# Optimization experiments

Hardware: AMD Instinct MI355X
Metric: run time of the kernel (lower is better)

The kernel has to match this reference:

```python
import jax, jax.numpy as jnp
import numpy as np

B, S, D, H = 8, 1024, 1024, 16
HD = D // H
EPS = 1e-5

def _layer_norm(x, g, b):
    m = jnp.mean(x, axis=-1, keepdims=True)
    v = jnp.var(x, axis=-1, keepdims=True)
    return (x - m) * jax.lax.rsqrt(v + EPS) * g + b

def setup_inputs() -> dict:
    key = jax.random.key(0)
    ks = jax.random.split(key, 12)
    s = lambda fan: 1.0 / np.sqrt(fan)
    return {
        "x": jax.random.normal(ks[0], (B, S, D), jnp.float32),
        "W_qkv": jax.random.normal(ks[1], (3 * D, D), jnp.float32) * s(D),
        "b_qkv": jnp.zeros((3 * D,), jnp.float32),
        "W_out": jax.random.normal(ks[2], (D, D), jnp.float32) * s(D),
        "b_out": jnp.zeros((D,), jnp.float32),
        "W1": jax.random.normal(ks[3], (2 * D, D), jnp.float32) * s(D),
        "b1": jnp.zeros((2 * D,), jnp.float32),
        "W2": jax.random.normal(ks[4], (D, 2 * D), jnp.float32) * s(2 * D),
        "b2": jnp.zeros((D,), jnp.float32),
        "ln1_g": jnp.ones((D,), jnp.float32),
        "ln1_b": jnp.zeros((D,), jnp.float32),
        "ln2_g": jnp.ones((D,), jnp.float32),
        "ln2_b": jnp.zeros((D,), jnp.float32),
    }

def reference(x, W_qkv, b_qkv, W_out, b_out, W1, b1, W2, b2, ln1_g, ln1_b, ln2_g, ln2_b):
    # --- self-attention (explicit, need_weights=True path) ---
    qkv = x @ W_qkv.T + b_qkv                       # [B,S,3D]
    q, k, v = jnp.split(qkv, 3, axis=-1)
    q = q.reshape(B, S, H, HD) * (1.0 / np.sqrt(HD))
    k = k.reshape(B, S, H, HD)
    v = v.reshape(B, S, H, HD)
    scores = jnp.einsum("bqhd,bkhd->bhqk", q, k)    # [B,H,S,S]
    probs = jax.nn.softmax(scores, axis=-1)          # materialized attn weights
    ctx = jnp.einsum("bhqk,bkhd->bqhd", probs, v).reshape(B, S, D)
    attn_out = ctx @ W_out.T + b_out
    # --- residual + LN, FFN, residual + LN ---
    x1 = _layer_norm(x + attn_out, ln1_g, ln1_b)
    ff = jax.nn.relu(x1 @ W1.T + b1) @ W2.T + b2
    x2 = _layer_norm(x1 + ff, ln2_g, ln2_b)
    return x2, probs
```

## Files before the change

kernel.cpp:

```cpp
#include <hip/hip_runtime.h>
#include <cstdint>

#define NB 8
#define NS 1024
#define ND 1024
#define NH 16
#define HD 64
static constexpr float LN_EPS = 1e-5f;

typedef unsigned short u16;
typedef short s16x8 __attribute__((ext_vector_type(8)));
typedef short s16x4 __attribute__((ext_vector_type(4)));
typedef float fx4   __attribute__((ext_vector_type(4)));

__device__ __forceinline__ u16 f2bf(float f) {
  union { float f; unsigned u; } v; v.f = f;
  return (u16)((v.u + 0x7fffu + ((v.u >> 16) & 1u)) >> 16);
}

__device__ __forceinline__ void gl_lds16(const void* g, void* lds) {
  __builtin_amdgcn_global_load_lds(
      (const __attribute__((address_space(1))) void*)g,
      (__attribute__((address_space(3))) void*)lds, 16, 0, 0);
}

__global__ __launch_bounds__(256) void cvt_f32_bf16(const float* __restrict__ in,
                                                    u16* __restrict__ out, int n4) {
  for (int i = blockIdx.x * 256 + threadIdx.x; i < n4; i += gridDim.x * 256) {
    const float4 v = reinterpret_cast<const float4*>(in)[i];
    s16x4 o;
    o[0] = (short)f2bf(v.x); o[1] = (short)f2bf(v.y);
    o[2] = (short)f2bf(v.z); o[3] = (short)f2bf(v.w);
    reinterpret_cast<s16x4*>(out)[i] = o;
  }
}

enum { EPI_SCORES = 0, EPI_QKV = 1, EPI_BIASRES = 2, EPI_FF1 = 3 };

template <int EPI>
__global__ __launch_bounds__(256, 2) void gemm_bt(
    const u16* __restrict__ A, const u16* __restrict__ B,
    const float* __restrict__ bias, const float* __restrict__ res,
    float* __restrict__ outF, u16* __restrict__ outB,
    u16* __restrict__ outQ, u16* __restrict__ outK, u16* __restrict__ outV,
    int M, int N, int K, long zsA, long zsB, long zsC) {
  __shared__ u16 sA[2][128 * 32];
  __shared__ u16 sB[2][128 * 32];
  const int t = threadIdx.x;
  const int lane = t & 63, wid = t >> 6;
  const int wm = wid >> 1, wn = wid & 1;
  const int z = blockIdx.z;
  A += (long)z * zsA;
  B += (long)z * zsB;
  const int tm0 = blockIdx.y * 128, tn0 = blockIdx.x * 128;
  const int nk = K >> 5;

  fx4 acc[4][4];
  const fx4 vzero = {0.f, 0.f, 0.f, 0.f};
#pragma unroll
  for (int i = 0; i < 4; ++i)
#pragma unroll
    for (int j = 0; j < 4; ++j) acc[i][j] = vzero;

  auto stage = [&](int buf, int kt) {
    const int k0 = kt << 5;
#pragma unroll
    for (int i = 0; i < 2; ++i) {
      const int e = (i * 256 + t) * 8;
      const int row = e >> 5, col = e & 31;
      gl_lds16(A + (long)(tm0 + row) * K + k0 + col, &sA[buf][e]);
    }
#pragma unroll
    for (int i = 0; i < 2; ++i) {
      const int e = (i * 256 + t) * 8;
      const int row = e >> 5, col = e & 31;
      gl_lds16(B + (long)(tn0 + row) * K + k0 + col, &sB[buf][e]);
    }
  };

  stage(0, 0);
  for (int kt = 0; kt < nk; ++kt) {
    const int cur = kt & 1;
    __syncthreads();
    if (kt + 1 < nk) stage(cur ^ 1, kt + 1);
    const int ar = wm * 64 + (lane & 15);
    const int br = wn * 64 + (lane & 15);
    const int kc = (lane >> 4) * 8;
    s16x8 a[4], b[4];
#pragma unroll
    for (int i = 0; i < 4; ++i) a[i] = *(const s16x8*)&sA[cur][(ar + i * 16) * 32 + kc];
#pragma unroll
    for (int i = 0; i < 4; ++i) b[i] = *(const s16x8*)&sB[cur][(br + i * 16) * 32 + kc];
#pragma unroll
    for (int mi = 0; mi < 4; ++mi)
#pragma unroll
      for (int ni = 0; ni < 4; ++ni)
        acc[mi][ni] = __builtin_amdgcn_mfma_f32_16x16x32_bf16(a[mi], b[ni], acc[mi][ni], 0, 0, 0);
  }

#pragma unroll
  for (int mi = 0; mi < 4; ++mi) {
#pragma unroll
    for (int ni = 0; ni < 4; ++ni) {
#pragma unroll
      for (int r = 0; r < 4; ++r) {
        const int row = tm0 + wm * 64 + mi * 16 + (lane >> 4) * 4 + r;
        const int col = tn0 + wn * 64 + ni * 16 + (lane & 15);
        float v = acc[mi][ni][r];
        if constexpr (EPI == EPI_SCORES) {
          outF[(long)z * zsC + (long)row * N + col] = v;
        } else if constexpr (EPI == EPI_QKV) {
          v += bias[col];
          const int bb = row >> 10, s = row & 1023;
          const int h = (col >> 6) & 15, d = col & 63;
          if (col < 1024)
            outQ[(((long)bb * NH + h) * NS + s) * HD + d] = f2bf(v * 0.125f);
          else if (col < 2048)
            outK[(((long)bb * NH + h) * NS + s) * HD + d] = f2bf(v);
          else
            outV[(((long)bb * NH + h) * HD + d) * NS + s] = f2bf(v);
        } else if constexpr (EPI == EPI_BIASRES) {
          v += bias[col] + res[(long)row * N + col];
          outF[(long)row * N + col] = v;
        } else {
          v += bias[col];
          v = v > 0.f ? v : 0.f;
          outB[(long)row * N + col] = f2bf(v);
        }
      }
    }
  }
}

__global__ __launch_bounds__(256, 2) void pv_gemm(const float* __restrict__ P,
                                                  const u16* __restrict__ Vt,
                                                  u16* __restrict__ ctxb) {
  __shared__ u16 sP[2][128 * 32];
  __shared__ u16 sV[2][64 * 32];
  const int t = threadIdx.x, lane = t & 63, w = t >> 6;
  const int z = blockIdx.y, bb = z >> 4, h = z & 15;
  const float* Pz = P + (long)z * (NS * NS);
  const u16* Vz = Vt + (long)z * (HD * NS);
  const int tm0 = blockIdx.x * 128;

  fx4 acc[2][4];
  const fx4 vzero = {0.f, 0.f, 0.f, 0.f};
#pragma unroll
  for (int i = 0; i < 2; ++i)
#pragma unroll
    for (int j = 0; j < 4; ++j) acc[i][j] = vzero;

  auto stage = [&](int buf, int kt) {
    const int k0 = kt << 5;
#pragma unroll
    for (int i = 0; i < 4; ++i) {
      const int e4 = (i * 256 + t) * 4;
      const int row = e4 >> 5, col = e4 & 31;
      const float4 v = *(const float4*)&Pz[(long)(tm0 + row) * NS + k0 + col];
      s16x4 o;
      o[0] = (short)f2bf(v.x); o[1] = (short)f2bf(v.y);
      o[2] = (short)f2bf(v.z); o[3] = (short)f2bf(v.w);
      *(s16x4*)&sP[buf][row * 32 + col] = o;
    }
    {
      const int e = t * 8;
      const int row = e >> 5, col = e & 31;
      gl_lds16(Vz + (long)row * NS + k0 + col, &sV[buf][e]);
    }
  };

  stage(0, 0);
  for (int kt = 0; kt < 32; ++kt) {
    const int cur = kt & 1;
    __syncthreads();
    if (kt + 1 < 32) stage(cur ^ 1, kt + 1);
    const int ar = w * 32 + (lane & 15);
    const int kc = (lane >> 4) * 8;
    s16x8 a[2], b[4];
#pragma unroll
    for (int i = 0; i < 2; ++i) a[i] = *(const s16x8*)&sP[cur][(ar + i * 16) * 32 + kc];
#pragma unroll
    for (int i = 0; i < 4; ++i) b[i] = *(const s16x8*)&sV[cur][(i * 16 + (lane & 15)) * 32 + kc];
#pragma unroll
    for (int mi = 0; mi < 2; ++mi)
#pragma unroll
      for (int ni = 0; ni < 4; ++ni)
        acc[mi][ni] = __builtin_amdgcn_mfma_f32_16x16x32_bf16(a[mi], b[ni], acc[mi][ni], 0, 0, 0);
  }

#pragma unroll
  for (int mi = 0; mi < 2; ++mi)
#pragma unroll
    for (int ni = 0; ni < 4; ++ni)
#pragma unroll
      for (int r = 0; r < 4; ++r) {
        const int row = tm0 + w * 32 + mi * 16 + (lane >> 4) * 4 + r;
        const int col = ni * 16 + (lane & 15);
        ctxb[((long)bb * NS + row) * ND + h * HD + col] = f2bf(acc[mi][ni][r]);
      }
}

__global__ __launch_bounds__(256) void softmax_rows(float* __restrict__ P) {
  float* p = P + (long)blockIdx.x * 1024;
  const int t = threadIdx.x, lane = t & 63, w = t >> 6;
  __shared__ float red[4];
  float4 v = *(float4*)&p[t * 4];
  float m = fmaxf(fmaxf(v.x, v.y), fmaxf(v.z, v.w));
#pragma unroll
  for (int o = 32; o >= 1; o >>= 1) m = fmaxf(m, __shfl_xor(m, o));
  if (lane == 0) red[w] = m;
  __syncthreads();
  m = fmaxf(fmaxf(red[0], red[1]), fmaxf(red[2], red[3]));
  v.x = __expf(v.x - m); v.y = __expf(v.y - m);
  v.z = __expf(v.z - m); v.w = __expf(v.w - m);
  float s = v.x + v.y + v.z + v.w;
#pragma unroll
  for (int o = 32; o >= 1; o >>= 1) s += __shfl_xor(s, o);
  __syncthreads();
  if (lane == 0) red[w] = s;
  __syncthreads();
  s = red[0] + red[1] + red[2] + red[3];
  const float inv = 1.0f / s;
  v.x *= inv; v.y *= inv; v.z *= inv; v.w *= inv;
  *(float4*)&p[t * 4] = v;
}

__global__ __launch_bounds__(256) void ln_rows(const float* __restrict__ Y,
                                               const float* __restrict__ g,
                                               const float* __restrict__ beta,
                                               float* __restrict__ outF,
                                               u16* __restrict__ outB) {
  const long row = blockIdx.x;
  const float* y = Y + row * 1024;
  const int t = threadIdx.x, lane = t & 63, w = t >> 6;
  __shared__ float rs_[4], rq_[4];
  const float4 v = *(const float4*)&y[t * 4];
  float s = v.x + v.y + v.z + v.w;
  float q = v.x * v.x + v.y * v.y + v.z * v.z + v.w * v.w;
#pragma unroll
  for (int o = 32; o >= 1; o >>= 1) { s += __shfl_xor(s, o); q += __shfl_xor(q, o); }
  if (lane == 0) { rs_[w] = s; rq_[w] = q; }
  __syncthreads();
  s = rs_[0] + rs_[1] + rs_[2] + rs_[3];
  q = rq_[0] + rq_[1] + rq_[2] + rq_[3];
  const float mean = s * (1.f / 1024.f);
  const float var = q * (1.f / 1024.f) - mean * mean;
  const float inv = rsqrtf(var + LN_EPS);
  const float4 gg = *(const float4*)&g[t * 4];
  const float4 bb = *(const float4*)&beta[t * 4];
  float o0 = (v.x - mean) * inv * gg.x + bb.x;
  float o1 = (v.y - mean) * inv * gg.y + bb.y;
  float o2 = (v.z - mean) * inv * gg.z + bb.z;
  float o3 = (v.w - mean) * inv * gg.w + bb.w;
  float4 ov; ov.x = o0; ov.y = o1; ov.z = o2; ov.w = o3;
  *(float4*)&outF[row * 1024 + t * 4] = ov;
  if (outB != nullptr) {
    s16x4 ob;
    ob[0] = (short)f2bf(o0); ob[1] = (short)f2bf(o1);
    ob[2] = (short)f2bf(o2); ob[3] = (short)f2bf(o3);
    *(s16x4*)&outB[row * 1024 + t * 4] = ob;
  }
}

extern "C" void kernel_launch(void* const* d_in, const int* in_sizes, int n_in,
                              void* d_out, int out_size, void* d_ws, size_t ws_size,
                              hipStream_t stream) {
  const float* x    = (const float*)d_in[0];
  const float* Wqkv = (const float*)d_in[1];
  const float* bqkv = (const float*)d_in[2];
  const float* Wout = (const float*)d_in[3];
  const float* bout = (const float*)d_in[4];
  const float* W1   = (const float*)d_in[5];
  const float* b1   = (const float*)d_in[6];
  const float* W2   = (const float*)d_in[7];
  const float* b2   = (const float*)d_in[8];
  const float* g1   = (const float*)d_in[9];
  const float* be1  = (const float*)d_in[10];
  const float* g2   = (const float*)d_in[11];
  const float* be2  = (const float*)d_in[12];

  float* x2    = (float*)d_out;
  float* probs = (float*)d_out + (long)NB * NS * ND;

  char* ws = (char*)d_ws;
  size_t off = 0;
  auto alloc = [&](size_t bytes) -> void* {
    void* p = ws + off;
    off += (bytes + 255) & ~(size_t)255;
    return p;
  };
  u16* xb   = (u16*)alloc((size_t)8192 * 1024 * 2);
  u16* wqb  = (u16*)alloc((size_t)3072 * 1024 * 2);
  u16* wob  = (u16*)alloc((size_t)1024 * 1024 * 2);
  u16* w1b  = (u16*)alloc((size_t)2048 * 1024 * 2);
  u16* w2b  = (u16*)alloc((size_t)1024 * 2048 * 2);
  u16* qb   = (u16*)alloc((size_t)NB * NH * NS * HD * 2);
  u16* kb   = (u16*)alloc((size_t)NB * NH * NS * HD * 2);
  u16* vb   = (u16*)alloc((size_t)NB * NH * HD * NS * 2);
  u16* ctxb = (u16*)alloc((size_t)8192 * 1024 * 2);
  float* yres = (float*)alloc((size_t)8192 * 1024 * 4);
  float* x1f  = (float*)alloc((size_t)8192 * 1024 * 4);
  u16* x1b  = (u16*)alloc((size_t)8192 * 1024 * 2);
  u16* h1b  = (u16*)alloc((size_t)8192 * 2048 * 2);

  cvt_f32_bf16<<<2048, 256, 0, stream>>>(x, xb, 8192 * 1024 / 4);
  cvt_f32_bf16<<<2048, 256, 0, stream>>>(Wqkv, wqb, 3072 * 1024 / 4);
  cvt_f32_bf16<<<512, 256, 0, stream>>>(Wout, wob, 1024 * 1024 / 4);
  cvt_f32_bf16<<<1024, 256, 0, stream>>>(W1, w1b, 2048 * 1024 / 4);
  cvt_f32_bf16<<<1024, 256, 0, stream>>>(W2, w2b, 1024 * 2048 / 4);

  gemm_bt<EPI_QKV><<<dim3(24, 64, 1), 256, 0, stream>>>(
      xb, wqb, bqkv, nullptr, nullptr, nullptr, qb, kb, vb, 8192, 3072, 1024, 0, 0, 0);

  gemm_bt<EPI_SCORES><<<dim3(8, 8, 128), 256, 0, stream>>>(
      qb, kb, nullptr, nullptr, probs, nullptr, nullptr, nullptr, nullptr,
      1024, 1024, 64, (long)NS * HD, (long)NS * HD, (long)NS * NS);

  softmax_rows<<<NB * NH * NS, 256, 0, stream>>>(probs);

  pv_gemm<<<dim3(8, 128), 256, 0, stream>>>(probs, vb, ctxb);

  gemm_bt<EPI_BIASRES><<<dim3(8, 64, 1), 256, 0, stream>>>(
      ctxb, wob, bout, x, yres, nullptr, nullptr, nullptr, nullptr, 8192, 1024, 1024, 0, 0, 0);

  ln_rows<<<8192, 256, 0, stream>>>(yres, g1, be1, x1f, x1b);

  gemm_bt<EPI_FF1><<<dim3(16, 64, 1), 256, 0, stream>>>(
      x1b, w1b, b1, nullptr, nullptr, h1b, nullptr, nullptr, nullptr, 8192, 2048, 1024, 0, 0, 0);

  gemm_bt<EPI_BIASRES><<<dim3(8, 64, 1), 256, 0, stream>>>(
      h1b, w2b, b2, x1f, yres, nullptr, nullptr, nullptr, nullptr, 8192, 1024, 2048, 0, 0, 0);

  ln_rows<<<8192, 256, 0, stream>>>(yres, g2, be2, x2, nullptr);
}
```

Before: 1.291 ms.

## Fuse scores, softmax and PV into one attention kernel; merge weight conversions

Replaces the separate QK^T GEMM, the row softmax and the PV GEMM with one kernel. Each block handles 16 query rows of one head and holds all 1024 scores in registers, so softmax runs in registers and the bf16 probabilities are staged in LDS for the PV product. The fp32 probs are written once instead of being written, re-read and rewritten, and PV no longer re-reads them from global memory, which removes much of the memory traffic. It also merges the five fp32-to-bf16 conversion launches into one kernel. The trade-offs are larger register and LDS use per block, and K/V tiles reloaded by each of the 64 query blocks per head.

```diff
diff --git a/kernel.cpp b/kernel.cpp
--- a/kernel.cpp
+++ b/kernel.cpp
@@ -24,18 +24,29 @@
       (__attribute__((address_space(3))) void*)lds, 16, 0, 0);
 }
 
-__global__ __launch_bounds__(256) void cvt_f32_bf16(const float* __restrict__ in,
-                                                    u16* __restrict__ out, int n4) {
-  for (int i = blockIdx.x * 256 + threadIdx.x; i < n4; i += gridDim.x * 256) {
-    const float4 v = reinterpret_cast<const float4*>(in)[i];
+__global__ __launch_bounds__(256) void cvt_all(
+    const float* __restrict__ s0, u16* __restrict__ d0, int n0,
+    const float* __restrict__ s1, u16* __restrict__ d1, int n1,
+    const float* __restrict__ s2, u16* __restrict__ d2, int n2,
+    const float* __restrict__ s3, u16* __restrict__ d3, int n3,
+    const float* __restrict__ s4, u16* __restrict__ d4, int n4) {
+  const int c0 = n0, c1 = c0 + n1, c2 = c1 + n2, c3 = c2 + n3, c4 = c3 + n4;
+  for (int i = blockIdx.x * 256 + threadIdx.x; i < c4; i += gridDim.x * 256) {
+    const float* s; u16* d; int j;
+    if (i < c0)      { s = s0; d = d0; j = i; }
+    else if (i < c1) { s = s1; d = d1; j = i - c0; }
+    else if (i < c2) { s = s2; d = d2; j = i - c1; }
+    else if (i < c3) { s = s3; d = d3; j = i - c2; }
+    else             { s = s4; d = d4; j = i - c3; }
+    const float4 v = reinterpret_cast<const float4*>(s)[j];
     s16x4 o;
     o[0] = (short)f2bf(v.x); o[1] = (short)f2bf(v.y);
     o[2] = (short)f2bf(v.z); o[3] = (short)f2bf(v.w);
-    reinterpret_cast<s16x4*>(out)[i] = o;
-  }
-}
-
-enum { EPI_SCORES = 0, EPI_QKV = 1, EPI_BIASRES = 2, EPI_FF1 = 3 };
+    reinterpret_cast<s16x4*>(d)[j] = o;
+  }
+}
+
+enum { EPI_QKV = 1, EPI_BIASRES = 2, EPI_FF1 = 3 };
 
 template <int EPI>
 __global__ __launch_bounds__(256, 2) void gemm_bt(
@@ -43,15 +54,12 @@
     const float* __restrict__ bias, const float* __restrict__ res,
     float* __restrict__ outF, u16* __restrict__ outB,
     u16* __restrict__ outQ, u16* __restrict__ outK, u16* __restrict__ outV,
-    int M, int N, int K, long zsA, long zsB, long zsC) {
+    int M, int N, int K) {
   __shared__ u16 sA[2][128 * 32];
   __shared__ u16 sB[2][128 * 32];
   const int t = threadIdx.x;
   const int lane = t & 63, wid = t >> 6;
   const int wm = wid >> 1, wn = wid & 1;
-  const int z = blockIdx.z;
-  A += (long)z * zsA;
-  B += (long)z * zsB;
   const int tm0 = blockIdx.y * 128, tn0 = blockIdx.x * 128;
   const int nk = K >> 5;
 
@@ -107,9 +115,7 @@
         const int row = tm0 + wm * 64 + mi * 16 + (lane >> 4) * 4 + r;
         const int col = tn0 + wn * 64 + ni * 16 + (lane & 15);
         float v = acc[mi][ni][r];
-        if constexpr (EPI == EPI_SCORES) {
-          outF[(long)z * zsC + (long)row * N + col] = v;
-        } else if constexpr (EPI == EPI_QKV) {
+        if constexpr (EPI == EPI_QKV) {
           v += bias[col];
           const int bb = row >> 10, s = row & 1023;
           const int h = (col >> 6) & 15, d = col & 63;
@@ -132,97 +138,149 @@
   }
 }
 
-__global__ __launch_bounds__(256, 2) void pv_gemm(const float* __restrict__ P,
-                                                  const u16* __restrict__ Vt,
-                                                  u16* __restrict__ ctxb) {
-  __shared__ u16 sP[2][128 * 32];
-  __shared__ u16 sV[2][64 * 32];
-  const int t = threadIdx.x, lane = t & 63, w = t >> 6;
-  const int z = blockIdx.y, bb = z >> 4, h = z & 15;
-  const float* Pz = P + (long)z * (NS * NS);
-  const u16* Vz = Vt + (long)z * (HD * NS);
-  const int tm0 = blockIdx.x * 128;
-
-  fx4 acc[2][4];
+__global__ __launch_bounds__(256, 2) void attn_fused(
+    const u16* __restrict__ qb, const u16* __restrict__ kb, const u16* __restrict__ vb,
+    float* __restrict__ probs, u16* __restrict__ ctxb) {
+  __shared__ u16 sK[2][64 * 64];
+  __shared__ u16 sV[2][64 * 64];
+  __shared__ u16 sP[16 * 1024];
+  __shared__ float redA[16][4], redB[16][4];
+  const int t = threadIdx.x, l = t & 63, w = t >> 6;
+  const int g = l >> 4, m = l & 15;
+  const int z = blockIdx.y;
+  const int q0 = blockIdx.x * 16;
+  const int bb = z >> 4, h = z & 15;
+  const u16* Qz = qb + (long)z * (NS * HD);
+  const u16* Kz = kb + (long)z * (NS * HD);
+  const u16* Vz = vb + (long)z * (HD * NS);
+
+  s16x8 qf[2];
+#pragma unroll
+  for (int kk = 0; kk < 2; ++kk)
+    qf[kk] = *(const s16x8*)&Qz[(q0 + m) * HD + kk * 32 + g * 8];
+
+  auto stageK = [&](int buf, int kt) {
+#pragma unroll
+    for (int i = 0; i < 2; ++i) {
+      const int a = (i * 256 + t) * 16;
+      const int row = a >> 7, off = a & 127;
+      const int soff = off ^ ((row & 7) << 4);
+      gl_lds16(Kz + (kt * 64 + row) * HD + (soff >> 1), (char*)&sK[buf][0] + a);
+    }
+  };
+  auto stageV = [&](int buf, int kt) {
+#pragma unroll
+    for (int i = 0; i < 2; ++i) {
+      const int a = (i * 256 + t) * 16;
+      const int row = a >> 7, off = a & 127;
+      const int soff = off ^ ((row & 7) << 4);
+      gl_lds16(Vz + (long)row * NS + kt * 64 + (soff >> 1), (char*)&sV[buf][0] + a);
+    }
+  };
+
+  fx4 sacc[16];
   const fx4 vzero = {0.f, 0.f, 0.f, 0.f};
 #pragma unroll
-  for (int i = 0; i < 2; ++i)
-#pragma unroll
-    for (int j = 0; j < 4; ++j) acc[i][j] = vzero;
-
-  auto stage = [&](int buf, int kt) {
-    const int k0 = kt << 5;
-#pragma unroll
-    for (int i = 0; i < 4; ++i) {
-      const int e4 = (i * 256 + t) * 4;
-      const int row = e4 >> 5, col = e4 & 31;
-      const float4 v = *(const float4*)&Pz[(long)(tm0 + row) * NS + k0 + col];
-      s16x4 o;
-      o[0] = (short)f2bf(v.x); o[1] = (short)f2bf(v.y);
-      o[2] = (short)f2bf(v.z); o[3] = (short)f2bf(v.w);
-      *(s16x4*)&sP[buf][row * 32 + col] = o;
-    }
-    {
-      const int e = t * 8;
-      const int row = e >> 5, col = e & 31;
-      gl_lds16(Vz + (long)row * NS + k0 + col, &sV[buf][e]);
-    }
-  };
-
-  stage(0, 0);
-  for (int kt = 0; kt < 32; ++kt) {
+  for (int i = 0; i < 16; ++i) sacc[i] = vzero;
+
+  stageK(0, 0);
+  for (int kt = 0; kt < 16; ++kt) {
     const int cur = kt & 1;
     __syncthreads();
-    if (kt + 1 < 32) stage(cur ^ 1, kt + 1);
-    const int ar = w * 32 + (lane & 15);
-    const int kc = (lane >> 4) * 8;
-    s16x8 a[2], b[4];
-#pragma unroll
-    for (int i = 0; i < 2; ++i) a[i] = *(const s16x8*)&sP[cur][(ar + i * 16) * 32 + kc];
-#pragma unroll
-    for (int i = 0; i < 4; ++i) b[i] = *(const s16x8*)&sV[cur][(i * 16 + (lane & 15)) * 32 + kc];
-#pragma unroll
-    for (int mi = 0; mi < 2; ++mi)
-#pragma unroll
-      for (int ni = 0; ni < 4; ++ni)
-        acc[mi][ni] = __builtin_amdgcn_mfma_f32_16x16x32_bf16(a[mi], b[ni], acc[mi][ni], 0, 0, 0);
-  }
-
-#pragma unroll
-  for (int mi = 0; mi < 2; ++mi)
-#pragma unroll
-    for (int ni = 0; ni < 4; ++ni)
-#pragma unroll
-      for (int r = 0; r < 4; ++r) {
-        const int row = tm0 + w * 32 + mi * 16 + (lane >> 4) * 4 + r;
-        const int col = ni * 16 + (lane & 15);
-        ctxb[((long)bb * NS + row) * ND + h * HD + col] = f2bf(acc[mi][ni][r]);
-      }
-}
-
-__global__ __launch_bounds__(256) void softmax_rows(float* __restrict__ P) {
-  float* p = P + (long)blockIdx.x * 1024;
-  const int t = threadIdx.x, lane = t & 63, w = t >> 6;
-  __shared__ float red[4];
-  float4 v = *(float4*)&p[t * 4];
-  float m = fmaxf(fmaxf(v.x, v.y), fmaxf(v.z, v.w));
-#pragma unroll
-  for (int o = 32; o >= 1; o >>= 1) m = fmaxf(m, __shfl_xor(m, o));
-  if (lane == 0) red[w] = m;
+    if (kt + 1 < 16) stageK(cur ^ 1, kt + 1);
+    const int krow = w * 16 + m;
+#pragma unroll
+    for (int kk = 0; kk < 2; ++kk) {
+      const s16x8 bf = *(const s16x8*)((const char*)&sK[cur][0] + krow * 128 +
+                                       ((kk * 64 + g * 16) ^ ((krow & 7) << 4)));
+      sacc[kt] = __builtin_amdgcn_mfma_f32_16x16x32_bf16(qf[kk], bf, sacc[kt], 0, 0, 0);
+    }
+  }
+
+  float rmax[4], rsum[4];
+#pragma unroll
+  for (int r = 0; r < 4; ++r) {
+    float mx = sacc[0][r];
+#pragma unroll
+    for (int i = 1; i < 16; ++i) mx = fmaxf(mx, sacc[i][r]);
+    mx = fmaxf(mx, __shfl_xor(mx, 1));
+    mx = fmaxf(mx, __shfl_xor(mx, 2));
+    mx = fmaxf(mx, __shfl_xor(mx, 4));
+    mx = fmaxf(mx, __shfl_xor(mx, 8));
+    rmax[r] = mx;
+  }
+  if (m == 0) {
+#pragma unroll
+    for (int r = 0; r < 4; ++r) redA[4 * g + r][w] = rmax[r];
+  }
   __syncthreads();
-  m = fmaxf(fmaxf(red[0], red[1]), fmaxf(red[2], red[3]));
-  v.x = __expf(v.x - m); v.y = __expf(v.y - m);
-  v.z = __expf(v.z - m); v.w = __expf(v.w - m);
-  float s = v.x + v.y + v.z + v.w;
-#pragma unroll
-  for (int o = 32; o >= 1; o >>= 1) s += __shfl_xor(s, o);
+#pragma unroll
+  for (int r = 0; r < 4; ++r) {
+    const float* rr = redA[4 * g + r];
+    rmax[r] = fmaxf(fmaxf(rr[0], rr[1]), fmaxf(rr[2], rr[3]));
+    rsum[r] = 0.f;
+  }
+#pragma unroll
+  for (int i = 0; i < 16; ++i)
+#pragma unroll
+    for (int r = 0; r < 4; ++r) {
+      const float e = __expf(sacc[i][r] - rmax[r]);
+      sacc[i][r] = e;
+      rsum[r] += e;
+    }
+#pragma unroll
+  for (int r = 0; r < 4; ++r) {
+    float s = rsum[r];
+    s += __shfl_xor(s, 1); s += __shfl_xor(s, 2);
+    s += __shfl_xor(s, 4); s += __shfl_xor(s, 8);
+    rsum[r] = s;
+  }
+  if (m == 0) {
+#pragma unroll
+    for (int r = 0; r < 4; ++r) redB[4 * g + r][w] = rsum[r];
+  }
   __syncthreads();
-  if (lane == 0) red[w] = s;
-  __syncthreads();
-  s = red[0] + red[1] + red[2] + red[3];
-  const float inv = 1.0f / s;
-  v.x *= inv; v.y *= inv; v.z *= inv; v.w *= inv;
-  *(float4*)&p[t * 4] = v;
+  float inv[4];
+#pragma unroll
+  for (int r = 0; r < 4; ++r) {
+    const float* rr = redB[4 * g + r];
+    inv[r] = 1.0f / (rr[0] + rr[1] + rr[2] + rr[3]);
+  }
+
+  float* Pz = probs + (long)z * (NS * NS);
+#pragma unroll
+  for (int i = 0; i < 16; ++i) {
+    const int col = i * 64 + w * 16 + m;
+#pragma unroll
+    for (int r = 0; r < 4; ++r) {
+      const int qr = 4 * g + r;
+      const float p = sacc[i][r] * inv[r];
+      Pz[(long)(q0 + qr) * NS + col] = p;
+      *(u16*)((char*)sP + qr * 2048 + ((col * 2) ^ ((qr & 7) << 4))) = f2bf(p);
+    }
+  }
+
+  fx4 cacc = vzero;
+  stageV(0, 0);
+  for (int kt = 0; kt < 16; ++kt) {
+    const int cur = kt & 1;
+    __syncthreads();
+    if (kt + 1 < 16) stageV(cur ^ 1, kt + 1);
+    const int d = w * 16 + m;
+#pragma unroll
+    for (int kk = 0; kk < 2; ++kk) {
+      const s16x8 af = *(const s16x8*)((const char*)sP + m * 2048 +
+                                       ((kt * 128 + kk * 64 + g * 16) ^ ((m & 7) << 4)));
+      const s16x8 bf = *(const s16x8*)((const char*)&sV[cur][0] + d * 128 +
+                                       ((kk * 64 + g * 16) ^ ((d & 7) << 4)));
+      cacc = __builtin_amdgcn_mfma_f32_16x16x32_bf16(af, bf, cacc, 0, 0, 0);
+    }
+  }
+#pragma unroll
+  for (int r = 0; r < 4; ++r) {
+    const int qr = 4 * g + r;
+    ctxb[((long)bb * NS + q0 + qr) * ND + h * HD + w * 16 + m] = f2bf(cacc[r]);
+  }
 }
 
 __global__ __launch_bounds__(256) void ln_rows(const float* __restrict__ Y,
@@ -303,33 +361,27 @@
   u16* x1b  = (u16*)alloc((size_t)8192 * 1024 * 2);
   u16* h1b  = (u16*)alloc((size_t)8192 * 2048 * 2);
 
-  cvt_f32_bf16<<<2048, 256, 0, stream>>>(x, xb, 8192 * 1024 / 4);
-  cvt_f32_bf16<<<2048, 256, 0, stream>>>(Wqkv, wqb, 3072 * 1024 / 4);
-  cvt_f32_bf16<<<512, 256, 0, stream>>>(Wout, wob, 1024 * 1024 / 4);
-  cvt_f32_bf16<<<1024, 256, 0, stream>>>(W1, w1b, 2048 * 1024 / 4);
-  cvt_f32_bf16<<<1024, 256, 0, stream>>>(W2, w2b, 1024 * 2048 / 4);
-
-  gemm_bt<EPI_QKV><<<dim3(24, 64, 1), 256, 0, stream>>>(
-      xb, wqb, bqkv, nullptr, nullptr, nullptr, qb, kb, vb, 8192, 3072, 1024, 0, 0, 0);
-
-  gemm_bt<EPI_SCORES><<<dim3(8, 8, 128), 256, 0, stream>>>(
-      qb, kb, nullptr, nullptr, probs, nullptr, nullptr, nullptr, nullptr,
-      1024, 1024, 64, (long)NS * HD, (long)NS * HD, (long)NS * NS);
-
-  softmax_rows<<<NB * NH * NS, 256, 0, stream>>>(probs);
-
-  pv_gemm<<<dim3(8, 128), 256, 0, stream>>>(probs, vb, ctxb);
-
-  gemm_bt<EPI_BIASRES><<<dim3(8, 64, 1), 256, 0, stream>>>(
-      ctxb, wob, bout, x, yres, nullptr, nullptr, nullptr, nullptr, 8192, 1024, 1024, 0, 0, 0);
+  cvt_all<<<2048, 256, 0, stream>>>(x, xb, 8192 * 1024 / 4,
+                                    Wqkv, wqb, 3072 * 1024 / 4,
+                                    Wout, wob, 1024 * 1024 / 4,
+                                    W1, w1b, 2048 * 1024 / 4,
+                                    W2, w2b, 2048 * 1024 / 4);
+
+  gemm_bt<EPI_QKV><<<dim3(24, 64), 256, 0, stream>>>(
+      xb, wqb, bqkv, nullptr, nullptr, nullptr, qb, kb, vb, 8192, 3072, 1024);
+
+  attn_fused<<<dim3(64, 128), 256, 0, stream>>>(qb, kb, vb, probs, ctxb);
+
+  gemm_bt<EPI_BIASRES><<<dim3(8, 64), 256, 0, stream>>>(
+      ctxb, wob, bout, x, yres, nullptr, nullptr, nullptr, nullptr, 8192, 1024, 1024);
 
   ln_rows<<<8192, 256, 0, stream>>>(yres, g1, be1, x1f, x1b);
 
-  gemm_bt<EPI_FF1><<<dim3(16, 64, 1), 256, 0, stream>>>(
-      x1b, w1b, b1, nullptr, nullptr, h1b, nullptr, nullptr, nullptr, 8192, 2048, 1024, 0, 0, 0);
-
-  gemm_bt<EPI_BIASRES><<<dim3(8, 64, 1), 256, 0, stream>>>(
-      h1b, w2b, b2, x1f, yres, nullptr, nullptr, nullptr, nullptr, 8192, 1024, 2048, 0, 0, 0);
+  gemm_bt<EPI_FF1><<<dim3(16, 64), 256, 0, stream>>>(
+      x1b, w1b, b1, nullptr, nullptr, h1b, nullptr, nullptr, nullptr, 8192, 2048, 1024);
+
+  gemm_bt<EPI_BIASRES><<<dim3(8, 64), 256, 0, stream>>>(
+      h1b, w2b, b2, x1f, yres, nullptr, nullptr, nullptr, nullptr, 8192, 1024, 2048);
 
   ln_rows<<<8192, 256, 0, stream>>>(yres, g2, be2, x2, nullptr);
 }
```

Measured after the change: 1.186 ms. 1.09x faster.
